# Kernel optimization log

Measured on AMD Instinct MI355X. Metric: run time of the kernel, lower is better.

Reference implementation:

```python
import jax, jax.numpy as jnp
import numpy as np

HIDDEN = 64
SEQ_LEN = 96
NUM_BASIS = 10
NUM_CLASSES = 2
IN_SIZE = 1
B = 16384


def _basis(x, W, a, c):
    # x: (B, in); a, c: (in, K); W: (in, out, K)
    # KAN-style ferroelectric basis: sum_{i,k} W[i,o,k] * tanh(a[i,k]*x[b,i] + c[i,k])
    phi = jnp.tanh(x[:, :, None] * a[None] + c[None])  # (B, in, K)
    return jnp.einsum('bik,iok->bo', phi, W)           # (B, out)


def setup_inputs() -> dict:
    key = jax.random.key(0)
    ks = jax.random.split(key, 11)
    s_in = 1.0 / np.sqrt(IN_SIZE * NUM_BASIS)
    s_h = 1.0 / np.sqrt(HIDDEN * NUM_BASIS)
    return {
        'x': jax.random.normal(ks[0], (B, SEQ_LEN), dtype=jnp.float32),
        'Wx': jax.random.normal(ks[1], (IN_SIZE, HIDDEN, NUM_BASIS), dtype=jnp.float32) * s_in,
        'ax': jax.random.normal(ks[2], (IN_SIZE, NUM_BASIS), dtype=jnp.float32),
        'cx': jax.random.normal(ks[3], (IN_SIZE, NUM_BASIS), dtype=jnp.float32),
        'Wh': jax.random.normal(ks[4], (HIDDEN, HIDDEN, NUM_BASIS), dtype=jnp.float32) * s_h,
        'ah': jax.random.normal(ks[5], (HIDDEN, NUM_BASIS), dtype=jnp.float32),
        'ch': jax.random.normal(ks[6], (HIDDEN, NUM_BASIS), dtype=jnp.float32),
        'Wc': jax.random.normal(ks[7], (HIDDEN, HIDDEN, NUM_BASIS), dtype=jnp.float32) * s_h,
        'ac': jax.random.normal(ks[8], (HIDDEN, NUM_BASIS), dtype=jnp.float32),
        'cc': jax.random.normal(ks[9], (HIDDEN, NUM_BASIS), dtype=jnp.float32),
        'Wout': jax.random.normal(ks[10], (HIDDEN, NUM_CLASSES), dtype=jnp.float32),
    }


def reference(x, Wx, ax, cx, Wh, ah, ch, Wc, ac, cc, Wout):
    Bsz = x.shape[0]

    def step(h, x_t):
        # x_t: (B,) -> (B, 1)
        x_phi = _basis(x_t[:, None], Wx, ax, cx)   # (B, HIDDEN)
        h_phi = _basis(h, Wh, ah, ch)              # (B, HIDDEN)
        comb = jnp.tanh(jnp.concatenate([x_phi, h_phi], axis=1))  # (B, 2H)
        return comb[:, :HIDDEN], None

    h0 = jnp.zeros((Bsz, HIDDEN), dtype=x.dtype)
    h, _ = jax.lax.scan(step, h0, jnp.transpose(x))  # scan over SEQ_LEN

    # KAN classifier head
    phi = jnp.tanh(_basis(h, Wc, ac, cc))  # (B, HIDDEN)
    return phi @ Wout                      # (B, NUM_CLASSES)
```

## Files before the change

### kernel.cpp

```cpp
#include <hip/hip_runtime.h>

#define HIDDEN 64
#define SEQLEN 96
#define NB 10
#define BATCH 16384
#define NCLASS 2
#define KTOT (HIDDEN * NB)
#define NKC (KTOT / 32)
#define MT 16
#define NW 4
#define KCW (NKC / NW)

typedef __attribute__((ext_vector_type(8))) short bf16x8;
typedef __attribute__((ext_vector_type(4))) float f32x4;

__device__ __forceinline__ float fast_tanh(float x) {
    float e = __expf(x + x);
    float r = __builtin_amdgcn_rcpf(e + 1.0f);
    return fmaf(-2.0f, r, 1.0f);
}

__device__ __forceinline__ unsigned bf16_rn(float f) {
    unsigned u = __float_as_uint(f);
    return (u + 0x8000u) >> 16;
}

__global__ __launch_bounds__(256) void prep_wb(const float* __restrict__ Wc,
                                               ushort* __restrict__ Wp) {
    int e = blockIdx.x * 256 + threadIdx.x;
    int j = e & 7;
    int lane = (e >> 3) & 63;
    int rest = e >> 9;
    int nt = rest & 3;
    int kcg = rest >> 2;
    int q = kcg * 32 + (lane >> 4) * 8 + j;
    int o = nt * 16 + (lane & 15);
    int i = q / 10;
    int k = q - i * 10;
    Wp[e] = (ushort)bf16_rn(Wc[i * (HIDDEN * NB) + o * NB + k]);
}

__global__ __launch_bounds__(256, 4) void kan_mfma(
    const float* __restrict__ x,
    const float* __restrict__ Wx,
    const float* __restrict__ ax, const float* __restrict__ cx,
    const float* __restrict__ ac,
    const float* __restrict__ cc,
    const float* __restrict__ Wout,
    const ushort* __restrict__ Wp,
    float* __restrict__ out)
{
    __shared__ float hs[65 * 16];
    __shared__ float Cred[16 * 64];
    __shared__ float outb[MT * NCLASS];

    const int lane = threadIdx.x;
    const int w    = threadIdx.y;
    const int tid  = w * 64 + lane;
    const int bb   = blockIdx.x * MT;

    for (int idx = tid; idx < 16 * 64; idx += 256) Cred[idx] = 0.0f;

    {
        const int sm = tid & 15;
        const int sg = tid >> 4;
        const float u = x[(bb + sm) * SEQLEN + (SEQLEN - 1)];
        float t[NB];
#pragma unroll
        for (int k = 0; k < NB; ++k)
            t[k] = fast_tanh(fmaf(ax[k], u, cx[k]));
#pragma unroll
        for (int r = 0; r < 4; ++r) {
            const int i = sg * 4 + r;
            const float* wxr = Wx + i * NB;
            float hx = 0.0f;
#pragma unroll
            for (int k = 0; k < NB; ++k)
                hx = fmaf(wxr[k], t[k], hx);
            hs[i * 16 + sm] = fast_tanh(hx);
        }
    }
    __syncthreads();

    const int m    = lane & 15;
    const int quad = lane >> 4;
    f32x4 acc0 = {0,0,0,0}, acc1 = {0,0,0,0}, acc2 = {0,0,0,0}, acc3 = {0,0,0,0};

#pragma unroll
    for (int c = 0; c < KCW; ++c) {
        const int kcg = w * KCW + c;
        const int q0  = kcg * 32 + quad * 8;
        const int i0  = q0 / 10;
        const int r0  = q0 - i0 * 10;
        const float h0 = hs[i0 * 16 + m];
        const float h1 = hs[(i0 + 1) * 16 + m];
        const float4 a0 = *(const float4*)(ac + q0);
        const float4 a1 = *(const float4*)(ac + q0 + 4);
        const float4 c0 = *(const float4*)(cc + q0);
        const float4 c1 = *(const float4*)(cc + q0 + 4);
        const float av[8] = {a0.x,a0.y,a0.z,a0.w,a1.x,a1.y,a1.z,a1.w};
        const float cv[8] = {c0.x,c0.y,c0.z,c0.w,c1.x,c1.y,c1.z,c1.w};
        float p[8];
#pragma unroll
        for (int j = 0; j < 8; ++j) {
            const float hj = (r0 + j >= 10) ? h1 : h0;
            p[j] = fast_tanh(fmaf(av[j], hj, cv[j]));
        }
        union { unsigned u[4]; bf16x8 v; } af;
#pragma unroll
        for (int jj = 0; jj < 4; ++jj)
            af.u[jj] = bf16_rn(p[2 * jj]) | (bf16_rn(p[2 * jj + 1]) << 16);

        const ushort* wb = Wp + (size_t)(kcg * 4) * 512 + lane * 8;
        const bf16x8 b0 = *(const bf16x8*)(wb);
        const bf16x8 b1 = *(const bf16x8*)(wb + 512);
        const bf16x8 b2 = *(const bf16x8*)(wb + 1024);
        const bf16x8 b3 = *(const bf16x8*)(wb + 1536);
        acc0 = __builtin_amdgcn_mfma_f32_16x16x32_bf16(af.v, b0, acc0, 0, 0, 0);
        acc1 = __builtin_amdgcn_mfma_f32_16x16x32_bf16(af.v, b1, acc1, 0, 0, 0);
        acc2 = __builtin_amdgcn_mfma_f32_16x16x32_bf16(af.v, b2, acc2, 0, 0, 0);
        acc3 = __builtin_amdgcn_mfma_f32_16x16x32_bf16(af.v, b3, acc3, 0, 0, 0);
    }

#pragma unroll
    for (int reg = 0; reg < 4; ++reg) {
        const int row = quad * 4 + reg;
        atomicAdd(&Cred[row * 64 +  0 + m], acc0[reg]);
        atomicAdd(&Cred[row * 64 + 16 + m], acc1[reg]);
        atomicAdd(&Cred[row * 64 + 32 + m], acc2[reg]);
        atomicAdd(&Cred[row * 64 + 48 + m], acc3[reg]);
    }
    __syncthreads();

    {
        const int mm = tid >> 4;
        const int ob = (tid & 15) * 4;
        float r0 = 0.0f, r1 = 0.0f;
#pragma unroll
        for (int t2 = 0; t2 < 4; ++t2) {
            const int o = ob + t2;
            const float g = fast_tanh(Cred[mm * 64 + o]);
            r0 = fmaf(g, Wout[o * NCLASS + 0], r0);
            r1 = fmaf(g, Wout[o * NCLASS + 1], r1);
        }
#pragma unroll
        for (int off = 8; off > 0; off >>= 1) {
            r0 += __shfl_down(r0, off, 16);
            r1 += __shfl_down(r1, off, 16);
        }
        if ((tid & 15) == 0) {
            outb[mm * NCLASS + 0] = r0;
            outb[mm * NCLASS + 1] = r1;
        }
    }
    __syncthreads();
    if (tid < MT * NCLASS)
        out[bb * NCLASS + tid] = outb[tid];
}

extern "C" void kernel_launch(void* const* d_in, const int* in_sizes, int n_in,
                              void* d_out, int out_size, void* d_ws, size_t ws_size,
                              hipStream_t stream) {
    const float* x    = (const float*)d_in[0];
    const float* Wx   = (const float*)d_in[1];
    const float* ax   = (const float*)d_in[2];
    const float* cx   = (const float*)d_in[3];
    const float* Wc   = (const float*)d_in[7];
    const float* ac   = (const float*)d_in[8];
    const float* cc   = (const float*)d_in[9];
    const float* Wout = (const float*)d_in[10];
    float* out  = (float*)d_out;
    ushort* Wp  = (ushort*)d_ws;

    prep_wb<<<dim3(NKC * 4 * 512 / 256), dim3(256), 0, stream>>>(Wc, Wp);
    kan_mfma<<<dim3(BATCH / MT), dim3(64, NW), 0, stream>>>(
        x, Wx, ax, cx, ac, cc, Wout, Wp, out);
}
```

Baseline: 102.0 us.

## Use five waves per block, per-wave reduction buffers, padded LDS, coalesced weight prep

The main kernel now runs 5 waves per block, each handling 4 of the 20 K-chunks, instead of 4 waves with 5 chunks each. LDS float atomics for the cross-wave reduction are replaced by plain stores into per-wave padded buffers, summed in the epilogue. The K loop is no longer unrolled, loads are issued before the tanh work, and the hs stride is padded to reduce bank conflicts. The weight prep kernel now reads Wc coalesced and scatters its writes. This trades extra LDS and a summation pass for removing atomics and spreading the K work across more waves.

```diff
diff --git a/kernel.cpp b/kernel.cpp
--- a/kernel.cpp
+++ b/kernel.cpp
@@ -8,8 +8,10 @@
 #define KTOT (HIDDEN * NB)
 #define NKC (KTOT / 32)
 #define MT 16
-#define NW 4
+#define NW 5
 #define KCW (NKC / NW)
+#define HSS 17
+#define CRS 66
 
 typedef __attribute__((ext_vector_type(8))) short bf16x8;
 typedef __attribute__((ext_vector_type(4))) float f32x4;
@@ -27,20 +29,19 @@
 
 __global__ __launch_bounds__(256) void prep_wb(const float* __restrict__ Wc,
                                                ushort* __restrict__ Wp) {
-    int e = blockIdx.x * 256 + threadIdx.x;
-    int j = e & 7;
-    int lane = (e >> 3) & 63;
-    int rest = e >> 9;
-    int nt = rest & 3;
-    int kcg = rest >> 2;
-    int q = kcg * 32 + (lane >> 4) * 8 + j;
-    int o = nt * 16 + (lane & 15);
-    int i = q / 10;
-    int k = q - i * 10;
-    Wp[e] = (ushort)bf16_rn(Wc[i * (HIDDEN * NB) + o * NB + k]);
+    const int e = blockIdx.x * 256 + threadIdx.x;
+    const float v = Wc[e];
+    const int i   = e / 640;
+    const int rem = e - i * 640;
+    const int o   = rem / 10;
+    const int k   = rem - o * 10;
+    const int q   = i * NB + k;
+    const int kcg = q >> 5, lhi = (q >> 3) & 3, j = q & 7;
+    const int nt  = o >> 4, n = o & 15;
+    Wp[(((kcg * 4 + nt) * 64) + lhi * 16 + n) * 8 + j] = (ushort)bf16_rn(v);
 }
 
-__global__ __launch_bounds__(256, 4) void kan_mfma(
+__global__ __launch_bounds__(64 * NW, 5) void kan_mfma(
     const float* __restrict__ x,
     const float* __restrict__ Wx,
     const float* __restrict__ ax, const float* __restrict__ cx,
@@ -50,8 +51,8 @@
     const ushort* __restrict__ Wp,
     float* __restrict__ out)
 {
-    __shared__ float hs[65 * 16];
-    __shared__ float Cred[16 * 64];
+    __shared__ float hs[65 * HSS];
+    __shared__ float Cred[NW][MT * CRS];
     __shared__ float outb[MT * NCLASS];
 
     const int lane = threadIdx.x;
@@ -59,9 +60,7 @@
     const int tid  = w * 64 + lane;
     const int bb   = blockIdx.x * MT;
 
-    for (int idx = tid; idx < 16 * 64; idx += 256) Cred[idx] = 0.0f;
-
-    {
+    if (tid < 256) {
         const int sm = tid & 15;
         const int sg = tid >> 4;
         const float u = x[(bb + sm) * SEQLEN + (SEQLEN - 1)];
@@ -77,69 +76,76 @@
 #pragma unroll
             for (int k = 0; k < NB; ++k)
                 hx = fmaf(wxr[k], t[k], hx);
-            hs[i * 16 + sm] = fast_tanh(hx);
+            hs[i * HSS + sm] = fast_tanh(hx);
         }
     }
     __syncthreads();
 
     const int m    = lane & 15;
     const int quad = lane >> 4;
-    f32x4 acc0 = {0,0,0,0}, acc1 = {0,0,0,0}, acc2 = {0,0,0,0}, acc3 = {0,0,0,0};
+    f32x4 a0 = {0,0,0,0}, a1 = {0,0,0,0}, a2 = {0,0,0,0}, a3 = {0,0,0,0};
 
-#pragma unroll
+#pragma unroll 1
     for (int c = 0; c < KCW; ++c) {
         const int kcg = w * KCW + c;
         const int q0  = kcg * 32 + quad * 8;
-        const int i0  = q0 / 10;
-        const int r0  = q0 - i0 * 10;
-        const float h0 = hs[i0 * 16 + m];
-        const float h1 = hs[(i0 + 1) * 16 + m];
-        const float4 a0 = *(const float4*)(ac + q0);
-        const float4 a1 = *(const float4*)(ac + q0 + 4);
-        const float4 c0 = *(const float4*)(cc + q0);
-        const float4 c1 = *(const float4*)(cc + q0 + 4);
-        const float av[8] = {a0.x,a0.y,a0.z,a0.w,a1.x,a1.y,a1.z,a1.w};
-        const float cv[8] = {c0.x,c0.y,c0.z,c0.w,c1.x,c1.y,c1.z,c1.w};
-        float p[8];
-#pragma unroll
-        for (int j = 0; j < 8; ++j) {
-            const float hj = (r0 + j >= 10) ? h1 : h0;
-            p[j] = fast_tanh(fmaf(av[j], hj, cv[j]));
-        }
-        union { unsigned u[4]; bf16x8 v; } af;
-#pragma unroll
-        for (int jj = 0; jj < 4; ++jj)
-            af.u[jj] = bf16_rn(p[2 * jj]) | (bf16_rn(p[2 * jj + 1]) << 16);
-
         const ushort* wb = Wp + (size_t)(kcg * 4) * 512 + lane * 8;
         const bf16x8 b0 = *(const bf16x8*)(wb);
         const bf16x8 b1 = *(const bf16x8*)(wb + 512);
         const bf16x8 b2 = *(const bf16x8*)(wb + 1024);
         const bf16x8 b3 = *(const bf16x8*)(wb + 1536);
-        acc0 = __builtin_amdgcn_mfma_f32_16x16x32_bf16(af.v, b0, acc0, 0, 0, 0);
-        acc1 = __builtin_amdgcn_mfma_f32_16x16x32_bf16(af.v, b1, acc1, 0, 0, 0);
-        acc2 = __builtin_amdgcn_mfma_f32_16x16x32_bf16(af.v, b2, acc2, 0, 0, 0);
-        acc3 = __builtin_amdgcn_mfma_f32_16x16x32_bf16(af.v, b3, acc3, 0, 0, 0);
+        const float4 av0 = *(const float4*)(ac + q0);
+        const float4 av1 = *(const float4*)(ac + q0 + 4);
+        const float4 cv0 = *(const float4*)(cc + q0);
+        const float4 cv1 = *(const float4*)(cc + q0 + 4);
+        const int i0 = q0 / 10;
+        const int r0 = q0 - i0 * 10;
+        const float h0 = hs[i0 * HSS + m];
+        const float h1 = hs[(i0 + 1) * HSS + m];
+
+        const float av[8] = {av0.x,av0.y,av0.z,av0.w,av1.x,av1.y,av1.z,av1.w};
+        const float cv[8] = {cv0.x,cv0.y,cv0.z,cv0.w,cv1.x,cv1.y,cv1.z,cv1.w};
+        union { unsigned u[4]; bf16x8 v; } af;
+#pragma unroll
+        for (int jj = 0; jj < 4; ++jj) {
+            const int j0 = 2 * jj, j1 = j0 + 1;
+            const float hj0 = (r0 + j0 >= 10) ? h1 : h0;
+            const float hj1 = (r0 + j1 >= 10) ? h1 : h0;
+            const float p0 = fast_tanh(fmaf(av[j0], hj0, cv[j0]));
+            const float p1 = fast_tanh(fmaf(av[j1], hj1, cv[j1]));
+            af.u[jj] = bf16_rn(p0) | (bf16_rn(p1) << 16);
+        }
+        a0 = __builtin_amdgcn_mfma_f32_16x16x32_bf16(af.v, b0, a0, 0, 0, 0);
+        a1 = __builtin_amdgcn_mfma_f32_16x16x32_bf16(af.v, b1, a1, 0, 0, 0);
+        a2 = __builtin_amdgcn_mfma_f32_16x16x32_bf16(af.v, b2, a2, 0, 0, 0);
+        a3 = __builtin_amdgcn_mfma_f32_16x16x32_bf16(af.v, b3, a3, 0, 0, 0);
     }
 
+    {
+        float* cr = Cred[w];
 #pragma unroll
-    for (int reg = 0; reg < 4; ++reg) {
-        const int row = quad * 4 + reg;
-        atomicAdd(&Cred[row * 64 +  0 + m], acc0[reg]);
-        atomicAdd(&Cred[row * 64 + 16 + m], acc1[reg]);
-        atomicAdd(&Cred[row * 64 + 32 + m], acc2[reg]);
-        atomicAdd(&Cred[row * 64 + 48 + m], acc3[reg]);
+        for (int reg = 0; reg < 4; ++reg) {
+            const int row = quad * 4 + reg;
+            cr[row * CRS +  0 + m] = a0[reg];
+            cr[row * CRS + 16 + m] = a1[reg];
+            cr[row * CRS + 32 + m] = a2[reg];
+            cr[row * CRS + 48 + m] = a3[reg];
+        }
     }
     __syncthreads();
 
-    {
+    if (tid < 256) {
         const int mm = tid >> 4;
         const int ob = (tid & 15) * 4;
         float r0 = 0.0f, r1 = 0.0f;
 #pragma unroll
         for (int t2 = 0; t2 < 4; ++t2) {
             const int o = ob + t2;
-            const float g = fast_tanh(Cred[mm * 64 + o]);
+            float s = 0.0f;
+#pragma unroll
+            for (int ww = 0; ww < NW; ++ww)
+                s += Cred[ww][mm * CRS + o];
+            const float g = fast_tanh(s);
             r0 = fmaf(g, Wout[o * NCLASS + 0], r0);
             r1 = fmaf(g, Wout[o * NCLASS + 1], r1);
         }
@@ -172,7 +178,7 @@
     float* out  = (float*)d_out;
     ushort* Wp  = (ushort*)d_ws;
 
-    prep_wb<<<dim3(NKC * 4 * 512 / 256), dim3(256), 0, stream>>>(Wc, Wp);
+    prep_wb<<<dim3(KTOT * HIDDEN / 256), dim3(256), 0, stream>>>(Wc, Wp);
     kan_mfma<<<dim3(BATCH / MT), dim3(64, NW), 0, stream>>>(
         x, Wx, ax, cx, ac, cc, Wout, Wp, out);
 }
```

Result: faster. 84.30 us (-17.3%).
